# Kernel optimization log

Hardware: AMD Instinct MI355X
Metric: run time of the kernel (lower is better)

## Reference

```python
import jax, jax.numpy as jnp
import numpy as np

N = 8192
VOCAB = 50000
EDIM = 256
WFEAT = 256
SLOPE = 0.01
NEG_INF = -1e9


def _gat_layer(x, adj, W, a_src, a_dst):
    # x: [N, Fin], adj: [N, N] (binary, self-loops included)
    h = x @ W                                   # [N, Fout]
    s = h @ a_src                               # [N] attention source term
    d = h @ a_dst                               # [N] attention dest term
    e = jax.nn.leaky_relu(s[:, None] + d[None, :], negative_slope=SLOPE)  # [N, N]
    e = jnp.where(adj > 0, e, NEG_INF)
    attn = jax.nn.softmax(e, axis=1)            # per-node softmax over neighbors
    out = attn @ h                              # scatter-aggregate
    return out, attn


def setup_inputs() -> dict:
    key = jax.random.key(0)
    ks = jax.random.split(key, 10)
    inDoc = jax.random.randint(ks[0], (N,), 0, VOCAB)
    p = 32.0 / N  # avg degree ~32
    eye = jnp.eye(N, dtype=jnp.float32)
    adj0 = jnp.clip(jax.random.bernoulli(ks[1], p, (N, N)).astype(jnp.float32) + eye, 0.0, 1.0)
    adj1 = jnp.clip(jax.random.bernoulli(ks[2], p, (N, N)).astype(jnp.float32) + eye, 0.0, 1.0)
    sc_e = 1.0 / np.sqrt(EDIM)
    sc_w = 1.0 / np.sqrt(WFEAT)
    emb = jax.random.normal(ks[3], (VOCAB, EDIM), dtype=jnp.float32) * sc_e
    W1 = jax.random.normal(ks[4], (EDIM, WFEAT), dtype=jnp.float32) * sc_e
    a1_src = jax.random.normal(ks[5], (WFEAT,), dtype=jnp.float32) * sc_w
    a1_dst = jax.random.normal(ks[6], (WFEAT,), dtype=jnp.float32) * sc_w
    W2 = jax.random.normal(ks[7], (WFEAT, WFEAT), dtype=jnp.float32) * sc_w
    a2_src = jax.random.normal(ks[8], (WFEAT,), dtype=jnp.float32) * sc_w
    a2_dst = jax.random.normal(ks[9], (WFEAT,), dtype=jnp.float32) * sc_w
    return {"inDoc": inDoc, "adj0": adj0, "adj1": adj1, "emb": emb,
            "W1": W1, "a1_src": a1_src, "a1_dst": a1_dst,
            "W2": W2, "a2_src": a2_src, "a2_dst": a2_dst}


def reference(inDoc, adj0, adj1, emb, W1, a1_src, a1_dst, W2, a2_src, a2_dst):
    words = emb[inDoc]                              # embedding lookup [N, EDIM]
    words, sattention = _gat_layer(words, adj0, W1, a1_src, a1_dst)
    document, dattention = _gat_layer(words, adj1, W2, a2_src, a2_dst)
    document = document + words                     # residual
    docMean = jnp.mean(document, axis=0)            # [WFEAT]
    return docMean, sattention, dattention
```

## Files before the change

### kernel.cpp

```cpp
#include <hip/hip_runtime.h>
#include <cstddef>

#define NN 8192
#define FD 256
#define LSLOPE 0.01f
#define NEGF -3.0e38f
#define CAP 96

typedef float f4 __attribute__((ext_vector_type(4)));

__global__ __launch_bounds__(256) void gemm_sd_kernel(
    const float* __restrict__ X,
    const int*   __restrict__ idx,
    const float* __restrict__ emb,
    const float* __restrict__ W,
    const float* __restrict__ a_src,
    const float* __restrict__ a_dst,
    float*       __restrict__ H,
    float*       __restrict__ s,
    float*       __restrict__ d)
{
    __shared__ __align__(16) float xs[16][FD];
    __shared__ __align__(16) f4    wbuf[2048];
    const int tid = threadIdx.x;
    const int n0  = blockIdx.x * 16;

    #pragma unroll
    for (int r = 0; r < 16; ++r) {
        const float* src = idx ? (emb + (size_t)idx[n0 + r] * FD)
                               : (X + (size_t)(n0 + r) * FD);
        xs[r][tid] = src[tid];
    }

    const int wave = tid >> 6;
    const int lane = tid & 63;
    const int c0 = lane * 4;
    const int r0 = wave * 4;
    const f4* W4 = reinterpret_cast<const f4*>(W);

    float acc[4][4] = {};
    for (int st = 0; st < FD / 32; ++st) {
        #pragma unroll
        for (int p = 0; p < 8; ++p)
            wbuf[p * 256 + tid] = W4[st * 2048 + p * 256 + tid];
        __syncthreads();

        #pragma unroll 4
        for (int kk = 0; kk < 32; ++kk) {
            const int k = st * 32 + kk;
            f4 w = wbuf[kk * 64 + lane];
            #pragma unroll
            for (int r = 0; r < 4; ++r) {
                float x = xs[r0 + r][k];
                acc[r][0] = fmaf(x, w[0], acc[r][0]);
                acc[r][1] = fmaf(x, w[1], acc[r][1]);
                acc[r][2] = fmaf(x, w[2], acc[r][2]);
                acc[r][3] = fmaf(x, w[3], acc[r][3]);
            }
        }
        __syncthreads();
    }

    const float4 as4 = *reinterpret_cast<const float4*>(a_src + c0);
    const float4 ad4 = *reinterpret_cast<const float4*>(a_dst + c0);

    #pragma unroll
    for (int r = 0; r < 4; ++r) {
        float4 o = make_float4(acc[r][0], acc[r][1], acc[r][2], acc[r][3]);
        *reinterpret_cast<float4*>(H + (size_t)(n0 + r0 + r) * FD + c0) = o;

        float ps = acc[r][0]*as4.x + acc[r][1]*as4.y + acc[r][2]*as4.z + acc[r][3]*as4.w;
        float pd = acc[r][0]*ad4.x + acc[r][1]*ad4.y + acc[r][2]*ad4.z + acc[r][3]*ad4.w;
        #pragma unroll
        for (int off = 32; off > 0; off >>= 1) {
            ps += __shfl_xor(ps, off);
            pd += __shfl_xor(pd, off);
        }
        if (lane == 0) {
            s[n0 + r0 + r] = ps;
            d[n0 + r0 + r] = pd;
        }
    }
}

__global__ __launch_bounds__(256, 6) void attn_compute_kernel(
    const float* __restrict__ adj,
    const float* __restrict__ svec,
    const float* __restrict__ dvec,
    const float* __restrict__ H,
    const float* residual,
    float* __restrict__ out_rows,
    int*   __restrict__ jw,
    float* __restrict__ pw,
    int*   __restrict__ nnzw,
    int list_base)
{
    __shared__ int   jbuf_s[4 * CAP];
    __shared__ float pbuf_s[4 * CAP];

    const int tid  = threadIdx.x;
    const int lane = tid & 63;
    const int wv   = tid >> 6;
    const int i    = blockIdx.x * 4 + wv;

    int*   jbuf = jbuf_s + wv * CAP;
    float* pbuf = pbuf_s + wv * CAP;

    const f4* arow4 = reinterpret_cast<const f4*>(adj + (size_t)i * NN);
    const unsigned long long lt = (lane == 0) ? 0ull : (~0ull >> (64 - lane));
    int base = 0;
    #pragma unroll
    for (int c = 0; c < 8; ++c) {
        f4 av[4];
        #pragma unroll
        for (int k = 0; k < 4; ++k)
            av[k] = __builtin_nontemporal_load(&arow4[c * 256 + k * 64 + lane]);
        #pragma unroll
        for (int k = 0; k < 4; ++k) {
            #pragma unroll
            for (int q = 0; q < 4; ++q) {
                const bool nz = (av[k][q] != 0.f);
                const unsigned long long mask = __ballot(nz);
                if (nz) {
                    const int pos = base + (int)__popcll(mask & lt);
                    if (pos < CAP)
                        jbuf[pos] = (c * 1024) + (k * 256) + (lane * 4) + q;
                }
                base += (int)__popcll(mask);
            }
        }
    }
    const int nnz = (base < CAP) ? base : CAP;

    const float si = svec[i];
    float mloc = NEGF;
    for (int t = lane; t < nnz; t += 64) {
        float e = si + dvec[jbuf[t]];
        e = (e >= 0.f) ? e : LSLOPE * e;
        pbuf[t] = e;
        mloc = fmaxf(mloc, e);
    }
    #pragma unroll
    for (int off = 32; off > 0; off >>= 1) mloc = fmaxf(mloc, __shfl_xor(mloc, off));
    const float m = mloc;

    float sloc = 0.f;
    for (int t = lane; t < nnz; t += 64) {
        float p = __expf(pbuf[t] - m);
        pbuf[t] = p;
        sloc += p;
    }
    #pragma unroll
    for (int off = 32; off > 0; off >>= 1) sloc += __shfl_xor(sloc, off);
    const float inv = 1.f / sloc;

    const size_t lrow = (size_t)(list_base + i) * CAP;
    for (int t = lane; t < nnz; t += 64) {
        jw[lrow + t] = jbuf[t];
        pw[lrow + t] = pbuf[t] * inv;
    }
    if (lane == 0) nnzw[list_base + i] = nnz;

    const f4* H4 = reinterpret_cast<const f4*>(H);
    f4 a0 = {0.f, 0.f, 0.f, 0.f};
    f4 a1 = {0.f, 0.f, 0.f, 0.f};
    f4 a2 = {0.f, 0.f, 0.f, 0.f};
    f4 a3 = {0.f, 0.f, 0.f, 0.f};
    int t = 0;
    for (; t + 4 <= nnz; t += 4) {
        a0 += pbuf[t]     * H4[(size_t)jbuf[t]     * 64 + lane];
        a1 += pbuf[t + 1] * H4[(size_t)jbuf[t + 1] * 64 + lane];
        a2 += pbuf[t + 2] * H4[(size_t)jbuf[t + 2] * 64 + lane];
        a3 += pbuf[t + 3] * H4[(size_t)jbuf[t + 3] * 64 + lane];
    }
    for (; t < nnz; ++t)
        a0 += pbuf[t] * H4[(size_t)jbuf[t] * 64 + lane];
    f4 o = ((a0 + a1) + (a2 + a3)) * inv;
    if (residual)
        o += reinterpret_cast<const f4*>(residual)[(size_t)i * 64 + lane];
    reinterpret_cast<f4*>(out_rows)[(size_t)i * 64 + lane] = o;
}

__global__ __launch_bounds__(256) void attn_expand_kernel(
    const int*   __restrict__ jw,
    const float* __restrict__ pw,
    const int*   __restrict__ nnzw,
    float* __restrict__ sattn,
    float* __restrict__ dattn)
{
    __shared__ __align__(16) float rbuf[NN];
    const int tid = threadIdx.x;
    const int row = blockIdx.x;

    f4* r4 = reinterpret_cast<f4*>(rbuf);
    const f4 z = {0.f, 0.f, 0.f, 0.f};
    #pragma unroll
    for (int g = 0; g < 8; ++g)
        r4[g * 256 + tid] = z;
    __syncthreads();

    const int nnz = nnzw[row];
    const size_t lrow = (size_t)row * CAP;
    for (int t = tid; t < nnz; t += 256)
        rbuf[jw[lrow + t]] = pw[lrow + t];
    __syncthreads();

    float* outp = (row < NN) ? (sattn + (size_t)row * NN)
                             : (dattn + (size_t)(row - NN) * NN);
    f4* o4 = reinterpret_cast<f4*>(outp);
    #pragma unroll
    for (int g = 0; g < 8; ++g)
        __builtin_nontemporal_store(r4[g * 256 + tid], &o4[g * 256 + tid]);
}

__global__ __launch_bounds__(256) void colsum_partial(
    const float* __restrict__ doc, float* __restrict__ partial)
{
    const int tid = threadIdx.x;
    const int b = blockIdx.x;
    float acc = 0.f;
    const float* p = doc + (size_t)b * 64 * FD + tid;
    #pragma unroll 8
    for (int r = 0; r < 64; ++r) acc += p[(size_t)r * FD];
    partial[b * FD + tid] = acc;
}

__global__ __launch_bounds__(256) void colsum_final(
    const float* __restrict__ partial, float* __restrict__ out)
{
    const int tid = threadIdx.x;
    float acc = 0.f;
    for (int b = 0; b < 128; ++b) acc += partial[b * FD + tid];
    out[tid] = acc * (1.f / (float)NN);
}

extern "C" void kernel_launch(void* const* d_in, const int* in_sizes, int n_in,
                              void* d_out, int out_size, void* d_ws, size_t ws_size,
                              hipStream_t stream)
{
    const int*   inDoc = (const int*)d_in[0];
    const float* adj0  = (const float*)d_in[1];
    const float* adj1  = (const float*)d_in[2];
    const float* emb   = (const float*)d_in[3];
    const float* W1    = (const float*)d_in[4];
    const float* a1s   = (const float*)d_in[5];
    const float* a1d   = (const float*)d_in[6];
    const float* W2    = (const float*)d_in[7];
    const float* a2s   = (const float*)d_in[8];
    const float* a2d   = (const float*)d_in[9];

    float* out     = (float*)d_out;
    float* docMean = out;
    float* sattn   = out + 256;
    float* dattn   = out + 256 + (size_t)NN * NN;

    float* ws = (float*)d_ws;
    float* h   = ws;
    float* o1  = ws + (size_t)NN * FD;
    float* s1  = ws + 2 * (size_t)NN * FD;
    float* d1  = s1 + NN;
    float* s2  = d1 + NN;
    float* d2  = s2 + NN;
    float* partial = d2 + NN;
    float* pw  = partial + 128 * FD;
    int*   jw  = (int*)(pw + (size_t)2 * NN * CAP);
    int*   nnzw = (int*)(jw + (size_t)2 * NN * CAP);

    gemm_sd_kernel<<<NN / 16, 256, 0, stream>>>(nullptr, inDoc, emb, W1, a1s, a1d, h, s1, d1);
    attn_compute_kernel<<<NN / 4, 256, 0, stream>>>(adj0, s1, d1, h, nullptr, o1,
                                                    jw, pw, nnzw, 0);

    gemm_sd_kernel<<<NN / 16, 256, 0, stream>>>(o1, nullptr, nullptr, W2, a2s, a2d, h, s2, d2);
    attn_compute_kernel<<<NN / 4, 256, 0, stream>>>(adj1, s2, d2, h, o1, o1,
                                                    jw, pw, nnzw, NN);

    colsum_partial<<<128, 256, 0, stream>>>(o1, partial);
    colsum_final<<<1, 256, 0, stream>>>(partial, docMean);

    attn_expand_kernel<<<2 * NN, 256, 0, stream>>>(jw, pw, nnzw, sattn, dattn);
}
```

Baseline: 296.4 us.

## Double-buffer adjacency row loads and replace per-element ballots with bitmask prefix scan

Result: slower. 304.2 us (+2.6%).

```diff
diff --git a/kernel.cpp b/kernel.cpp
--- a/kernel.cpp
+++ b/kernel.cpp
@@ -83,12 +83,12 @@
     }
 }
 
-__global__ __launch_bounds__(256, 6) void attn_compute_kernel(
+__global__ __launch_bounds__(256, 4) void attn_compute_kernel(
     const float* __restrict__ adj,
     const float* __restrict__ svec,
     const float* __restrict__ dvec,
     const float* __restrict__ H,
-    const float* residual,
+    const float* __restrict__ residual,
     float* __restrict__ out_rows,
     int*   __restrict__ jw,
     float* __restrict__ pw,
@@ -107,38 +107,92 @@
     float* pbuf = pbuf_s + wv * CAP;
 
     const f4* arow4 = reinterpret_cast<const f4*>(adj + (size_t)i * NN);
-    const unsigned long long lt = (lane == 0) ? 0ull : (~0ull >> (64 - lane));
-    int base = 0;
-    #pragma unroll
-    for (int c = 0; c < 8; ++c) {
-        f4 av[4];
-        #pragma unroll
-        for (int k = 0; k < 4; ++k)
-            av[k] = __builtin_nontemporal_load(&arow4[c * 256 + k * 64 + lane]);
-        #pragma unroll
-        for (int k = 0; k < 4; ++k) {
-            #pragma unroll
-            for (int q = 0; q < 4; ++q) {
-                const bool nz = (av[k][q] != 0.f);
-                const unsigned long long mask = __ballot(nz);
-                if (nz) {
-                    const int pos = base + (int)__popcll(mask & lt);
-                    if (pos < CAP)
-                        jbuf[pos] = (c * 1024) + (k * 256) + (lane * 4) + q;
-                }
-                base += (int)__popcll(mask);
-            }
-        }
-    }
-    const int nnz = (base < CAP) ? base : CAP;
+    f4 bufA[8], bufB[8];
+    unsigned int mask[4];
+
+    #pragma unroll
+    for (int k = 0; k < 8; ++k)
+        bufA[k] = __builtin_nontemporal_load(&arow4[(0 * 8 + k) * 64 + lane]);
+    #pragma unroll
+    for (int k = 0; k < 8; ++k)
+        bufB[k] = __builtin_nontemporal_load(&arow4[(1 * 8 + k) * 64 + lane]);
+
+    {
+        unsigned int m0 = 0;
+        #pragma unroll
+        for (int k = 0; k < 8; ++k)
+            #pragma unroll
+            for (int q = 0; q < 4; ++q)
+                m0 |= (bufA[k][q] != 0.f ? 1u : 0u) << (k * 4 + q);
+        mask[0] = m0;
+    }
+    #pragma unroll
+    for (int k = 0; k < 8; ++k)
+        bufA[k] = __builtin_nontemporal_load(&arow4[(2 * 8 + k) * 64 + lane]);
+
+    {
+        unsigned int m1 = 0;
+        #pragma unroll
+        for (int k = 0; k < 8; ++k)
+            #pragma unroll
+            for (int q = 0; q < 4; ++q)
+                m1 |= (bufB[k][q] != 0.f ? 1u : 0u) << (k * 4 + q);
+        mask[1] = m1;
+    }
+    #pragma unroll
+    for (int k = 0; k < 8; ++k)
+        bufB[k] = __builtin_nontemporal_load(&arow4[(3 * 8 + k) * 64 + lane]);
+
+    {
+        unsigned int m2 = 0;
+        #pragma unroll
+        for (int k = 0; k < 8; ++k)
+            #pragma unroll
+            for (int q = 0; q < 4; ++q)
+                m2 |= (bufA[k][q] != 0.f ? 1u : 0u) << (k * 4 + q);
+        mask[2] = m2;
+    }
+    {
+        unsigned int m3 = 0;
+        #pragma unroll
+        for (int k = 0; k < 8; ++k)
+            #pragma unroll
+            for (int q = 0; q < 4; ++q)
+                m3 |= (bufB[k][q] != 0.f ? 1u : 0u) << (k * 4 + q);
+        mask[3] = m3;
+    }
+
+    const int cnt = __popc(mask[0]) + __popc(mask[1])
+                  + __popc(mask[2]) + __popc(mask[3]);
+    int x = cnt;
+    #pragma unroll
+    for (int off = 1; off < 64; off <<= 1) {
+        int y = __shfl_up(x, off);
+        if (lane >= off) x += y;
+    }
+    int pos = x - cnt;
+    const int total = __shfl(x, 63);
+    const int nnz = (total < CAP) ? total : CAP;
 
     const float si = svec[i];
     float mloc = NEGF;
-    for (int t = lane; t < nnz; t += 64) {
-        float e = si + dvec[jbuf[t]];
-        e = (e >= 0.f) ? e : LSLOPE * e;
-        pbuf[t] = e;
-        mloc = fmaxf(mloc, e);
+    #pragma unroll
+    for (int w = 0; w < 4; ++w) {
+        unsigned int mw = mask[w];
+        while (mw) {
+            const int b = __builtin_ctz(mw);
+            mw &= mw - 1;
+            const int g = w * 8 + (b >> 2);
+            const int j = g * 256 + lane * 4 + (b & 3);
+            if (pos < CAP) {
+                float e = si + dvec[j];
+                e = (e >= 0.f) ? e : LSLOPE * e;
+                jbuf[pos] = j;
+                pbuf[pos] = e;
+                mloc = fmaxf(mloc, e);
+            }
+            ++pos;
+        }
     }
     #pragma unroll
     for (int off = 32; off > 0; off >>= 1) mloc = fmaxf(mloc, __shfl_xor(mloc, off));
@@ -257,7 +311,8 @@
     float* ws = (float*)d_ws;
     float* h   = ws;
     float* o1  = ws + (size_t)NN * FD;
-    float* s1  = ws + 2 * (size_t)NN * FD;
+    float* o2  = ws + 2 * (size_t)NN * FD;
+    float* s1  = ws + 3 * (size_t)NN * FD;
     float* d1  = s1 + NN;
     float* s2  = d1 + NN;
     float* d2  = s2 + NN;
@@ -266,15 +321,17 @@
     int*   jw  = (int*)(pw + (size_t)2 * NN * CAP);
     int*   nnzw = (int*)(jw + (size_t)2 * NN * CAP);
 
-    gemm_sd_kernel<<<NN / 16, 256, 0, stream>>>(nullptr, inDoc, emb, W1, a1s, a1d, h, s1, d1);
+    gemm_sd_kernel<<<NN / 16, 256, 0, stream>>>(nullptr, inDoc, emb, W1, a1s, a1d,
+                                                h, s1, d1);
     attn_compute_kernel<<<NN / 4, 256, 0, stream>>>(adj0, s1, d1, h, nullptr, o1,
                                                     jw, pw, nnzw, 0);
 
-    gemm_sd_kernel<<<NN / 16, 256, 0, stream>>>(o1, nullptr, nullptr, W2, a2s, a2d, h, s2, d2);
-    attn_compute_kernel<<<NN / 4, 256, 0, stream>>>(adj1, s2, d2, h, o1, o1,
+    gemm_sd_kernel<<<NN / 16, 256, 0, stream>>>(o1, nullptr, nullptr, W2, a2s, a2d,
+                                                h, s2, d2);
+    attn_compute_kernel<<<NN / 4, 256, 0, stream>>>(adj1, s2, d2, h, o1, o2,
                                                     jw, pw, nnzw, NN);
 
-    colsum_partial<<<128, 256, 0, stream>>>(o1, partial);
+    colsum_partial<<<128, 256, 0, stream>>>(o2, partial);
     colsum_final<<<1, 256, 0, stream>>>(partial, docMean);
 
     attn_expand_kernel<<<2 * NN, 256, 0, stream>>>(jw, pw, nnzw, sattn, dattn);
```
